# Performance work log

Hardware: AMD Instinct MI355X
Metric: run time of the kernel (lower is better)

## Reference

```python
import jax, jax.numpy as jnp
import numpy as np
from jax import lax

H, W = 14, 14          # spatial input_size
K = 6                  # mask_size (square)
ST = 2                 # mask_stride
_xs = np.arange(0, H - K + 1, ST)   # mask/window positions; (H-K)%ST==0 so grid matches avg_pool2d
M = len(_xs)
# pairwise rectangle-intersection coordinates between mask R1 (index a) and window W2 (index b)
_lo = np.maximum(_xs[:, None], _xs[None, :])                       # [M,M]
_hi = np.maximum(np.minimum(_xs[:, None] + K, _xs[None, :] + K), _lo)  # [M,M], clamped (empty -> zero area)


def setup_inputs() -> dict:
    key = jax.random.key(0)
    x = jax.random.normal(key, (32, 1000, H, W), dtype=jnp.float32)
    return {"x": x}


def _forward(x):
    B, C = x.shape[0], x.shape[1]
    total = jnp.sum(x, axis=(2, 3))  # [B,C]  == unmasked_logits
    # window sums == avg_pool2d(divisor_override=1); also equals sum over each mask region R1
    winsum = lax.reduce_window(x, 0.0, lax.add, (1, 1, K, K), (1, 1, ST, ST), 'VALID')  # [B,C,M,M]
    one_mask_logits = total[:, :, None, None] - winsum                # [B,C,M,M]
    one_mask_pred = jnp.argmax(one_mask_logits, axis=1)               # [B,M,M]
    pred = jnp.argmax(total, axis=1)                                  # [B]
    disagree = one_mask_pred != pred[:, None, None]                   # [B,M,M]

    # summed-area table for O(1) rectangle sums (zero-padded)
    sat = jnp.pad(jnp.cumsum(jnp.cumsum(x, axis=2), axis=3), ((0, 0), (0, 0), (1, 0), (1, 0)))
    xhi = _hi[:, None, :, None]; xlo = _lo[:, None, :, None]          # depend on (i, k)
    yhi = _hi[None, :, None, :]; ylo = _lo[None, :, None, :]          # depend on (j, l)
    # sum of x over R1(i,j) ∩ W2(k,l): [B,C,M,M,M,M]
    overlap = (sat[:, :, xhi, yhi] - sat[:, :, xlo, yhi]
               - sat[:, :, xhi, ylo] + sat[:, :, xlo, ylo])

    # two-mask logits: total - sum(R1) - sum(W2) + sum(R1 ∩ W2)
    two = (total[:, :, None, None, None, None]
           - winsum[:, :, :, :, None, None]
           - winsum[:, :, None, None, :, :]
           + overlap)                                                 # [B,C,M,M,M,M]
    two_pred = jnp.argmax(two, axis=1)                                # [B,M,M,M,M]

    # a disagreer (i,j) is confirmed if ALL second-mask preds equal its one-mask pred
    agree = jnp.all(two_pred == one_mask_pred[:, :, :, None, None], axis=(3, 4))  # [B,M,M]
    cand = (disagree & agree).reshape(B, -1)                          # row-major (i,j) order
    first = jnp.argmax(cand, axis=1)                                  # first confirmed disagreer
    new_pred = jnp.take_along_axis(one_mask_pred.reshape(B, -1), first[:, None], axis=1)[:, 0]
    pred = jnp.where(jnp.any(cand, axis=1), new_pred, pred)
    return pred, one_mask_logits


def reference(x):
    pred, _ = _forward(x)
    return pred
```

## Files before the change

### kernel.cpp

```cpp
#include <hip/hip_runtime.h>


#define NC 1000
#define NCH 16
#define PSTRIDE 384

__host__ __device__ constexpr int tri_off(int p) { return p * 25 - p * (p - 1) / 2; }

__global__ __launch_bounds__(384) void kernB(const float* __restrict__ x,
                                             unsigned long long* __restrict__ part) {
    __shared__ float lx[64 * 197];
    __shared__ float W[64][27];
    const int tid = threadIdx.x;
    const int b = blockIdx.x >> 4;
    const int wc = blockIdx.x & 15;
    const int c0 = (wc == 15) ? 936 : wc * 64;
    const int cl = tid & 63;
    const int hi = tid >> 6;

    const float4* x4 = reinterpret_cast<const float4*>(x)
                       + (size_t)(b * NC + c0) * 49;
#pragma unroll
    for (int it = 0; it < 9; ++it) {
        const int f = it * 384 + tid;
        if (f < 3136) {
            float4 v = x4[f];
            const int img = f / 49;
            const int off = f - img * 49;
            float* d = &lx[img * 197 + off * 4];
            d[0] = v.x; d[1] = v.y; d[2] = v.z; d[3] = v.w;
        }
    }
    __syncthreads();

    if (tid < 64) {
        float* row = &lx[tid * 197];
        float colacc[7];
#pragma unroll
        for (int c = 0; c < 7; ++c) colacc[c] = 0.f;
#pragma unroll
        for (int r = 0; r < 7; ++r) {
            float rowf[28];
#pragma unroll
            for (int j = 0; j < 28; ++j) rowf[j] = row[r * 28 + j];
            if (r == 0) {
#pragma unroll
                for (int j = 0; j < 8; ++j) row[j] = 0.f;
            }
            row[(r + 1) * 8] = 0.f;
            float run = 0.f;
#pragma unroll
            for (int c = 0; c < 7; ++c) {
                const float blk2 = rowf[2 * c] + rowf[2 * c + 1]
                                 + rowf[14 + 2 * c] + rowf[14 + 2 * c + 1];
                colacc[c] += blk2;
                run += colacc[c];
                row[(r + 1) * 8 + c + 1] = run;
            }
        }
    }
    __syncthreads();

#define SC(c, k) lx[(c) * 197 + (k)]
#pragma unroll
    for (int j = hi; j < 27; j += 6) {
        float v;
        if (j < 25) {
            const int p1 = j / 5, p2 = j % 5;
            v = ((SC(cl, (p1 + 3) * 8 + p2 + 3) - SC(cl, p1 * 8 + p2 + 3))
                 - SC(cl, (p1 + 3) * 8 + p2)) + SC(cl, p1 * 8 + p2);
        } else if (j == 25) {
            v = SC(cl, 63);
        } else {
            v = 0.f;
        }
        W[cl][j] = v;
    }
    __syncthreads();

    const int sid = tid;
    if (sid < 351) {
        int pi, qi, i0, i1, i2, i3;
        if (sid < 325) {
            int p = 0;
            while (tri_off(p + 1) <= sid) ++p;
            const int q = p + (sid - tri_off(p));
            const int p1 = p / 5, p2 = p % 5, q1 = q / 5, q2 = q % 5;
            const int rlo = (p1 > q1 ? p1 : q1);
            const int rmn = (p1 < q1 ? p1 : q1);
            const int rhi = (rmn + 3 > rlo ? rmn + 3 : rlo);
            const int clo = (p2 > q2 ? p2 : q2);
            const int cmn = (p2 < q2 ? p2 : q2);
            const int chi = (cmn + 3 > clo ? cmn + 3 : clo);
            pi = p; qi = q;
            i0 = rhi * 8 + chi; i1 = rlo * 8 + chi;
            i2 = rhi * 8 + clo; i3 = rlo * 8 + clo;
        } else if (sid < 350) {
            pi = sid - 325; qi = 26;
            i0 = i1 = i2 = i3 = 0;
        } else {
            pi = 26; qi = 26; i0 = i1 = i2 = i3 = 0;
        }
        float bv = -3.4e38f;
        int bc = 0;
#pragma unroll 4
        for (int c = 0; c < 64; ++c) {
            const float rect = ((SC(c, i0) - SC(c, i1)) - SC(c, i2)) + SC(c, i3);
            const float v = ((W[c][25] - W[c][pi]) - W[c][qi]) + rect;
            if (v > bv) { bv = v; bc = c; }
        }
        const unsigned u = __float_as_uint(bv);
        const unsigned fk = u ^ (unsigned)(((int)u >> 31) | 0x80000000);
        part[(size_t)(b * NCH + wc) * PSTRIDE + sid] =
            ((unsigned long long)fk << 32) | (unsigned)~(unsigned)(c0 + bc);
    }
#undef SC
}

__global__ __launch_bounds__(128) void kernC(const unsigned long long* __restrict__ part,
                                             int* __restrict__ out) {
    __shared__ unsigned long long mg[352];
    const int b = blockIdx.x;
    const int t = threadIdx.x;
    for (int s = t; s < 351; s += 128) {
        unsigned long long m = 0ull;
#pragma unroll
        for (int wc = 0; wc < NCH; ++wc) {
            unsigned long long v = part[(size_t)(b * NCH + wc) * PSTRIDE + s];
            if (v > m) m = v;
        }
        mg[s] = m;
    }
    __syncthreads();
    if (t < 64) {
        const unsigned predidx = (unsigned)mg[350];
        const int pred = (int)~predidx;
        bool cand = false;
        int p1 = 0;
        if (t < 25) {
            const unsigned p1i = (unsigned)mg[325 + t];
            p1 = (int)~p1i;
            bool ag = true;
            for (int j = 0; j < 25; ++j) {
                const int a = t < j ? t : j;
                const int q = t < j ? j : t;
                ag = ag && ((unsigned)mg[tri_off(a) + (q - a)] == p1i);
            }
            cand = ag && (p1 != pred);
        }
        const unsigned long long mask = __ballot(cand);
        int ans = pred;
        if (mask) ans = __shfl(p1, __ffsll(mask) - 1, 64);
        if (t == 0) out[b] = ans;
    }
}

extern "C" void kernel_launch(void* const* d_in, const int* in_sizes, int n_in,
                              void* d_out, int out_size, void* d_ws, size_t ws_size,
                              hipStream_t stream) {
    const float* x = (const float*)d_in[0];
    int* out = (int*)d_out;

    unsigned long long* part = (unsigned long long*)d_ws;

    kernB<<<32 * NCH, 384, 0, stream>>>(x, part);
    kernC<<<32, 128, 0, stream>>>(part, out);
}
```

Measured before the change: 83.03 us.

## Fuse reduction kernel into main kernel via last-block atomic counter

Merges the per-batch merge/decision kernel into the main kernel. Each block increments a per-batch atomic counter, and the last block for a batch reduces the partial argmax results and writes the prediction. It also precomputes total-minus-window sums into a second shared table, removing one subtraction per inner-loop iteration. The change adds a memset launch, threadfences, an atomic and extra shared memory, which could reduce occupancy.

```diff
diff --git a/kernel.cpp b/kernel.cpp
--- a/kernel.cpp
+++ b/kernel.cpp
@@ -4,13 +4,19 @@
 #define NC 1000
 #define NCH 16
 #define PSTRIDE 384
+#define PART_BYTES ((size_t)32 * NCH * PSTRIDE * 8)
 
 __host__ __device__ constexpr int tri_off(int p) { return p * 25 - p * (p - 1) / 2; }
 
-__global__ __launch_bounds__(384) void kernB(const float* __restrict__ x,
-                                             unsigned long long* __restrict__ part) {
+__global__ __launch_bounds__(384) void fused(const float* __restrict__ x,
+                                             unsigned long long* __restrict__ part,
+                                             int* __restrict__ cnt,
+                                             int* __restrict__ out) {
     __shared__ float lx[64 * 197];
     __shared__ float W[64][27];
+    __shared__ float LT[64][27];
+    __shared__ unsigned long long mg[352];
+    __shared__ int is_last;
     const int tid = threadIdx.x;
     const int b = blockIdx.x >> 4;
     const int wc = blockIdx.x & 15;
@@ -62,19 +68,24 @@
     __syncthreads();
 
 #define SC(c, k) lx[(c) * 197 + (k)]
+    {
+        const float total = SC(cl, 63);
 #pragma unroll
-    for (int j = hi; j < 27; j += 6) {
-        float v;
-        if (j < 25) {
-            const int p1 = j / 5, p2 = j % 5;
-            v = ((SC(cl, (p1 + 3) * 8 + p2 + 3) - SC(cl, p1 * 8 + p2 + 3))
-                 - SC(cl, (p1 + 3) * 8 + p2)) + SC(cl, p1 * 8 + p2);
-        } else if (j == 25) {
-            v = SC(cl, 63);
-        } else {
-            v = 0.f;
+        for (int j = hi; j < 27; j += 6) {
+            float wv, ltv;
+            if (j < 25) {
+                const int p1 = j / 5, p2 = j % 5;
+                wv = ((SC(cl, (p1 + 3) * 8 + p2 + 3) - SC(cl, p1 * 8 + p2 + 3))
+                      - SC(cl, (p1 + 3) * 8 + p2)) + SC(cl, p1 * 8 + p2);
+                ltv = total - wv;
+            } else if (j == 25) {
+                wv = total; ltv = total;
+            } else {
+                wv = 0.f; ltv = total;
+            }
+            W[cl][j] = wv;
+            LT[cl][j] = ltv;
         }
-        W[cl][j] = v;
     }
     __syncthreads();
 
@@ -99,14 +110,14 @@
             pi = sid - 325; qi = 26;
             i0 = i1 = i2 = i3 = 0;
         } else {
-            pi = 26; qi = 26; i0 = i1 = i2 = i3 = 0;
+            pi = 25; qi = 26; i0 = i1 = i2 = i3 = 0;
         }
         float bv = -3.4e38f;
         int bc = 0;
 #pragma unroll 4
         for (int c = 0; c < 64; ++c) {
             const float rect = ((SC(c, i0) - SC(c, i1)) - SC(c, i2)) + SC(c, i3);
-            const float v = ((W[c][25] - W[c][pi]) - W[c][qi]) + rect;
+            const float v = (LT[c][pi] - W[c][qi]) + rect;
             if (v > bv) { bv = v; bc = c; }
         }
         const unsigned u = __float_as_uint(bv);
@@ -115,35 +126,36 @@
             ((unsigned long long)fk << 32) | (unsigned)~(unsigned)(c0 + bc);
     }
 #undef SC
-}
 
-__global__ __launch_bounds__(128) void kernC(const unsigned long long* __restrict__ part,
-                                             int* __restrict__ out) {
-    __shared__ unsigned long long mg[352];
-    const int b = blockIdx.x;
-    const int t = threadIdx.x;
-    for (int s = t; s < 351; s += 128) {
+    __threadfence();
+    if (tid == 0)
+        is_last = (atomicAdd(&cnt[b], 1) == NCH - 1);
+    __syncthreads();
+    if (!is_last) return;
+    __threadfence();
+
+    if (tid < 351) {
         unsigned long long m = 0ull;
 #pragma unroll
-        for (int wc = 0; wc < NCH; ++wc) {
-            unsigned long long v = part[(size_t)(b * NCH + wc) * PSTRIDE + s];
+        for (int ch = 0; ch < NCH; ++ch) {
+            unsigned long long v = part[(size_t)(b * NCH + ch) * PSTRIDE + tid];
             if (v > m) m = v;
         }
-        mg[s] = m;
+        mg[tid] = m;
     }
     __syncthreads();
-    if (t < 64) {
+    if (tid < 64) {
         const unsigned predidx = (unsigned)mg[350];
         const int pred = (int)~predidx;
         bool cand = false;
         int p1 = 0;
-        if (t < 25) {
-            const unsigned p1i = (unsigned)mg[325 + t];
+        if (tid < 25) {
+            const unsigned p1i = (unsigned)mg[325 + tid];
             p1 = (int)~p1i;
             bool ag = true;
             for (int j = 0; j < 25; ++j) {
-                const int a = t < j ? t : j;
-                const int q = t < j ? j : t;
+                const int a = tid < j ? tid : j;
+                const int q = tid < j ? j : tid;
                 ag = ag && ((unsigned)mg[tri_off(a) + (q - a)] == p1i);
             }
             cand = ag && (p1 != pred);
@@ -151,7 +163,7 @@
         const unsigned long long mask = __ballot(cand);
         int ans = pred;
         if (mask) ans = __shfl(p1, __ffsll(mask) - 1, 64);
-        if (t == 0) out[b] = ans;
+        if (tid == 0) out[b] = ans;
     }
 }
 
@@ -160,9 +172,9 @@
                               hipStream_t stream) {
     const float* x = (const float*)d_in[0];
     int* out = (int*)d_out;
+    unsigned long long* part = (unsigned long long*)d_ws;
+    int* cnt = (int*)((char*)d_ws + PART_BYTES);
 
-    unsigned long long* part = (unsigned long long*)d_ws;
-
-    kernB<<<32 * NCH, 384, 0, stream>>>(x, part);
-    kernC<<<32, 128, 0, stream>>>(part, out);
+    hipMemsetAsync(cnt, 0, 32 * sizeof(int), stream);
+    fused<<<32 * NCH, 384, 0, stream>>>(x, part, cnt, out);
 }
```

Result: slower. 156.4 us (+88.4%).
